# Kernel tuning notes

Hardware: AMD Instinct MI355X
Metric: run time of the kernel (lower is better)

The kernel has to match this reference:

```python
import jax, jax.numpy as jnp
import numpy as np

N_SRC, N_TGT, N_EDGES = 100000, 50000, 1000000
S_IN, T_IN, S_OUT, T_OUT = 128, 128, 64, 64
NEG_SLOPE = 0.2


def setup_inputs() -> dict:
    key = jax.random.key(0)
    ks = jax.random.split(key, 7)
    return {
        "x_source": jax.random.normal(ks[0], (N_SRC, S_IN), jnp.float32),
        "x_target": jax.random.normal(ks[1], (N_TGT, T_IN), jnp.float32),
        "w_s": jax.random.normal(ks[2], (S_IN, T_OUT), jnp.float32) * 0.1,
        "w_t": jax.random.normal(ks[3], (T_IN, S_OUT), jnp.float32) * 0.1,
        "att_weight": jax.random.normal(ks[4], (T_OUT + S_OUT,), jnp.float32) * 0.1,
        "nbhd_values": jnp.ones((N_EDGES,), jnp.float32),
        "rows": jax.random.randint(ks[5], (N_EDGES,), 0, N_TGT, jnp.int32),  # target idx i
        "cols": jax.random.randint(ks[6], (N_EDGES,), 0, N_SRC, jnp.int32),  # source idx j
    }


def reference(x_source, x_target, w_s, w_t, att_weight, nbhd_values, rows, cols):
    n_src, n_tgt = x_source.shape[0], x_target.shape[0]
    t_out = w_s.shape[1]  # dim of s_message
    s_out = w_t.shape[1]  # dim of t_message

    s_msg = x_source @ w_s  # [n_src, t_out]
    t_msg = x_target @ w_t  # [n_tgt, s_out]

    # e_{ij} = LeakyReLU([s_msg_j || t_msg_i] . a); a = [a_s (t_out) || a_t (s_out)]
    a_s, a_t = att_weight[:t_out], att_weight[t_out:]
    # f uses permuted attention vector: [a[s_out:] || a[:s_out]] on [t_msg_j || s_msg_i]
    b_t, b_s = att_weight[s_out:], att_weight[:s_out]

    es = s_msg @ a_s  # [n_src]
    et = t_msg @ a_t  # [n_tgt]
    ft = t_msg @ b_t  # [n_tgt]
    fs = s_msg @ b_s  # [n_src]

    # s->t attention: rows are target cells (row-normalize over target rows)
    e = jax.nn.leaky_relu(es[cols] + et[rows], NEG_SLOPE)  # [E]
    e_den = jax.ops.segment_sum(e, rows, num_segments=n_tgt)
    att_st = e / e_den[rows]

    # t->s attention: transposed indices; rows are source cells
    f = jax.nn.leaky_relu(ft[rows] + fs[cols], NEG_SLOPE)  # [E]
    f_den = jax.ops.segment_sum(f, cols, num_segments=n_src)
    att_ts = f / f_den[cols]

    # Hadamard with neighborhood values, then sparse-dense aggregation
    w_st = att_st * nbhd_values  # [E]
    w_ts = att_ts * nbhd_values  # [E]

    message_on_target = jax.ops.segment_sum(w_st[:, None] * s_msg[cols], rows, num_segments=n_tgt)  # [n_tgt, t_out]
    message_on_source = jax.ops.segment_sum(w_ts[:, None] * t_msg[rows], cols, num_segments=n_src)  # [n_src, s_out]

    # update_func is None -> identity
    return message_on_source, message_on_target
```

## Files before the change

### kernel.cpp

```cpp
#include <hip/hip_runtime.h>

#define N_SRC   100000
#define N_TGT   50000
#define N_EDGES 1000000
#define NEG     0.2
#define NXCD    8
#define TPART   (N_TGT / NXCD)
#define SPART   (N_SRC / NXCD)

#define GBLK_S  1563
#define GBLK_T  782
#define GBLK    (GBLK_S + GBLK_T)
#define NHIST   1280


#define XS2 65
__global__ __launch_bounds__(256) void fused_gemm_hist(
    const float* __restrict__ x_source, const float* __restrict__ x_target,
    const float* __restrict__ w_s, const float* __restrict__ w_t,
    const float* __restrict__ att,
    float* __restrict__ s_msg, float* __restrict__ t_msg,
    double* __restrict__ es_d, double* __restrict__ et_d,
    const int* __restrict__ rows, const int* __restrict__ cols,
    int* __restrict__ cnt_r, int* __restrict__ cnt_c,
    int* __restrict__ rank_r, int* __restrict__ rank_c)
{
    __shared__ float xs[64 * XS2];
    __shared__ double eds[4][64];
    const int tid = threadIdx.x;

    if (blockIdx.x < NHIST) {
        for (int i = blockIdx.x * 256 + tid; i < N_EDGES; i += NHIST * 256) {
            rank_r[i] = atomicAdd(&cnt_r[rows[i]], 1);
            rank_c[i] = atomicAdd(&cnt_c[cols[i]], 1);
        }
        return;
    }

    const int gi = blockIdx.x - NHIST;

    const float* x; const float* w; int att_off, nrows, bblk;
    float* msg; double* evec;
    if (gi < GBLK_S) { x = x_source; w = w_s; att_off = 0;  nrows = N_SRC;
                       msg = s_msg;  evec = es_d; bblk = gi; }
    else             { x = x_target; w = w_t; att_off = 64; nrows = N_TGT;
                       msg = t_msg;  evec = et_d; bblk = gi - GBLK_S; }

    const int lane = tid & 63;
    const int part = tid >> 6;
    const int c0   = __builtin_amdgcn_readfirstlane(part << 4);
    const int row0 = bblk * 64;
    const int row  = row0 + lane;
    const bool act = row < nrows;

    float acc[16];
    #pragma unroll
    for (int c = 0; c < 16; ++c) acc[c] = 0.f;

    const int xbase = lane * XS2;

    #pragma unroll
    for (int h = 0; h < 2; ++h) {
        __syncthreads();
        #pragma unroll
        for (int it = 0; it < 4; ++it) {
            const int fid = tid + it * 256;
            const int r = fid >> 4, q = fid & 15;
            if (row0 + r < nrows) {
                const float4 v =
                    *(const float4*)(x + (size_t)(row0 + r) * 128 + h * 64 + 4 * q);
                float* d = &xs[r * XS2 + 4 * q];
                d[0] = v.x; d[1] = v.y; d[2] = v.z; d[3] = v.w;
            }
        }
        __syncthreads();

        for (int kc = 0; kc < 64; kc += 16) {
            #pragma unroll
            for (int kk = 0; kk < 16; ++kk) {
                const float xk = xs[xbase + kc + kk];
                const float* wr = w + (size_t)(h * 64 + kc + kk) * 64 + c0;
                #pragma unroll
                for (int c = 0; c < 16; ++c)
                    acc[c] = fmaf(xk, wr[c], acc[c]);
            }
        }
    }

    double e = 0.0;
    #pragma unroll
    for (int c = 0; c < 16; ++c)
        e += (double)acc[c] * (double)att[att_off + c0 + c];
    eds[part][lane] = e;
    __syncthreads();
    if (part == 0 && act)
        evec[row] = eds[0][lane] + eds[1][lane] + eds[2][lane] + eds[3][lane];

    if (act) {
        float* mo = msg + (size_t)row * 64 + c0;
        #pragma unroll
        for (int q = 0; q < 4; ++q)
            *(float4*)(mo + 4 * q) = *(float4*)(acc + 4 * q);
    }
}

__global__ __launch_bounds__(1024) void scan_two(
    const int* __restrict__ cnt_r, const int* __restrict__ cnt_c,
    int* __restrict__ ptr_r, int* __restrict__ ptr_c)
{
    const int n    = blockIdx.x ? N_SRC : N_TGT;
    const int* cnt = blockIdx.x ? cnt_c : cnt_r;
    int* ptr       = blockIdx.x ? ptr_c : ptr_r;
    const int tid  = threadIdx.x;
    const int lane = tid & 63, wid = tid >> 6;

    __shared__ int wsum[16];
    __shared__ int s_carry;
    if (tid == 0) s_carry = 0;
    __syncthreads();

    for (int base = 0; base < n; base += 4096) {
        const int idx = base + tid * 4;
        int4 v = make_int4(0, 0, 0, 0);
        if (idx + 3 < n) {
            v = *(const int4*)(cnt + idx);
        } else if (idx < n) {
            v.x = cnt[idx];
            if (idx + 1 < n) v.y = cnt[idx + 1];
            if (idx + 2 < n) v.z = cnt[idx + 2];
        }
        const int s = v.x + v.y + v.z + v.w;

        int p = s;
        #pragma unroll
        for (int d = 1; d < 64; d <<= 1) {
            int t = __shfl_up(p, d);
            if (lane >= d) p += t;
        }
        if (lane == 63) wsum[wid] = p;
        __syncthreads();
        if (tid == 0) {
            int a = 0;
            #pragma unroll
            for (int i = 0; i < 16; ++i) { int t = wsum[i]; wsum[i] = a; a += t; }
        }
        __syncthreads();

        int run = s_carry + wsum[wid] + (p - s);
        if (idx     < n) ptr[idx]     = run; run += v.x;
        if (idx + 1 < n) ptr[idx + 1] = run; run += v.y;
        if (idx + 2 < n) ptr[idx + 2] = run; run += v.z;
        if (idx + 3 < n) ptr[idx + 3] = run; run += v.w;

        __syncthreads();
        if (tid == 1023) s_carry = run;
        __syncthreads();
    }
    if (tid == 0) ptr[n] = s_carry;
}

__global__ __launch_bounds__(256) void scatter_part(
    const int* __restrict__ rows, const int* __restrict__ cols,
    const float* __restrict__ nbhd,
    const int* __restrict__ ptr_r, const int* __restrict__ ptr_c,
    const int* __restrict__ rank_r, const int* __restrict__ rank_c,
    unsigned long long* __restrict__ srtT, unsigned long long* __restrict__ srtS)
{
    const int xcd  = blockIdx.x & (NXCD - 1);
    const int ibx  = blockIdx.x >> 3;
    const int step = (gridDim.x >> 3) * blockDim.x;
    const int lo_r = xcd * TPART, lo_c = xcd * SPART;

    for (int i = ibx * blockDim.x + threadIdx.x; i < N_EDGES; i += step) {
        const int r = rows[i], c = cols[i];
        const bool mr = (unsigned)(r - lo_r) < TPART;
        const bool mc = (unsigned)(c - lo_c) < SPART;
        if (!(mr | mc)) continue;
        const unsigned long long nb =
            (unsigned long long)(unsigned)__float_as_int(nbhd[i]) << 32;
        if (mr) srtT[ptr_r[r] + rank_r[i]] = nb | (unsigned)c;
        if (mc) srtS[ptr_c[c] + rank_c[i]] = nb | (unsigned)r;
    }
}

__global__ __launch_bounds__(256) void gather_both(
    const int2* __restrict__ srtT, const int* __restrict__ ptr_r,
    const float* __restrict__ s_msg, float* __restrict__ msg_tgt,
    const int2* __restrict__ srtS, const int* __restrict__ ptr_c,
    const float* __restrict__ t_msg, float* __restrict__ msg_src,
    const double* __restrict__ es_d, const double* __restrict__ et_d)
{
    const int gw   = (blockIdx.x * blockDim.x + threadIdx.x) >> 6;
    const int lane = threadIdx.x & 63;

    const int2* srt; const int* ptr; const float* min_; float* out;
    const double* other_d; double base; int row;
    if (gw < N_TGT) {
        srt = srtT; ptr = ptr_r; min_ = s_msg; out = msg_tgt;
        other_d = es_d; row = gw; base = et_d[row];
    } else {
        row = gw - N_TGT;
        if (row >= N_SRC) return;
        srt = srtS; ptr = ptr_c; min_ = t_msg; out = msg_src;
        other_d = et_d; base = es_d[row];
    }

    const int b = ptr[row], e = ptr[row + 1];
    double den = 0.0;
    float a0 = 0.f, a1 = 0.f, a2 = 0.f, a3 = 0.f;

    for (int j0 = b; j0 < e; j0 += 64) {
        const int m = e - j0;
        int oidx = 0; double v = 0.0; float wf = 0.f;
        if (lane < m) {
            const int2 pay = srt[j0 + lane];
            oidx = pay.x;
            const float nb = __int_as_float(pay.y);
            const double sv = base + other_d[oidx];
            v = (sv >= 0.0) ? sv : NEG * sv;
            wf = (float)(v * (double)nb);
        }
        den += v;

        const int cnt = m < 64 ? m : 64;
        int j = 0;
        for (; j + 3 < cnt; j += 4) {
            const int   c0_ = __shfl(oidx, j);     const float w0 = __shfl(wf, j);
            const int   c1_ = __shfl(oidx, j + 1); const float w1 = __shfl(wf, j + 1);
            const int   c2_ = __shfl(oidx, j + 2); const float w2 = __shfl(wf, j + 2);
            const int   c3_ = __shfl(oidx, j + 3); const float w3 = __shfl(wf, j + 3);
            a0 = fmaf(w0, min_[(size_t)c0_ * 64 + lane], a0);
            a1 = fmaf(w1, min_[(size_t)c1_ * 64 + lane], a1);
            a2 = fmaf(w2, min_[(size_t)c2_ * 64 + lane], a2);
            a3 = fmaf(w3, min_[(size_t)c3_ * 64 + lane], a3);
        }
        for (; j < cnt; ++j) {
            const int   c = __shfl(oidx, j);
            const float w = __shfl(wf, j);
            a0 = fmaf(w, min_[(size_t)c * 64 + lane], a0);
        }
    }
    #pragma unroll
    for (int s = 32; s; s >>= 1) den += __shfl_xor(den, s);
    const double inv = (den != 0.0) ? 1.0 / den : 0.0;
    const double acc = (double)((a0 + a1) + (a2 + a3));
    out[(size_t)row * 64 + lane] = (float)(acc * inv);
}

extern "C" void kernel_launch(void* const* d_in, const int* in_sizes, int n_in,
                              void* d_out, int out_size, void* d_ws, size_t ws_size,
                              hipStream_t stream)
{
    const float* x_source = (const float*)d_in[0];
    const float* x_target = (const float*)d_in[1];
    const float* w_s      = (const float*)d_in[2];
    const float* w_t      = (const float*)d_in[3];
    const float* att      = (const float*)d_in[4];
    const float* nbhd     = (const float*)d_in[5];
    const int*   rows     = (const int*)d_in[6];
    const int*   cols     = (const int*)d_in[7];

    float* out     = (float*)d_out;
    float* msg_src = out;
    float* msg_tgt = out + (size_t)N_SRC * 64;

    char* ws = (char*)d_ws;
    float*  s_msg  = (float*) (ws + 0);
    float*  t_msg  = (float*) (ws + 25600000);
    double* es_d   = (double*)(ws + 38400000);
    double* et_d   = (double*)(ws + 39200000);
    int*    cnt_r  = (int*)   (ws + 39600000);
    int*    cnt_c  = (int*)   (ws + 39800000);
    int*    ptr_r  = (int*)   (ws + 40200000);
    int*    ptr_c  = (int*)   (ws + 40400004);
    int*    rank_r = (int*)   (ws + 40800016);
    int*    rank_c = (int*)   (ws + 44800016);
    unsigned long long* srtT = (unsigned long long*)(ws + 48800016);
    unsigned long long* srtS = (unsigned long long*)(ws + 56800016);

    hipMemsetAsync(ws + 39600000, 0, 600000, stream);

    fused_gemm_hist<<<NHIST + GBLK, 256, 0, stream>>>(
        x_source, x_target, w_s, w_t, att,
        s_msg, t_msg, es_d, et_d,
        rows, cols, cnt_r, cnt_c, rank_r, rank_c);

    scan_two<<<2, 1024, 0, stream>>>(cnt_r, cnt_c, ptr_r, ptr_c);
    scatter_part<<<2048, 256, 0, stream>>>(
        rows, cols, nbhd, ptr_r, ptr_c, rank_r, rank_c, srtT, srtS);

    gather_both<<<(N_TGT + N_SRC + 3) / 4, 256, 0, stream>>>(
        (const int2*)srtT, ptr_r, s_msg, msg_tgt,
        (const int2*)srtS, ptr_c, t_msg, msg_src, es_d, et_d);
}
```

Baseline: 297.5 us.

## Prefetch second GEMM half, unroll histogram atomics, and use nontemporal payload loads

The histogram blocks are halved, and each thread now issues four edges' loads and atomics before storing ranks, which gives more memory-level parallelism per thread. The GEMM path prefetches the second 64-column half of each x row into registers while the first half is being computed, so the global load latency between halves is hidden. The gather kernel reads the sorted payload as 64-bit nontemporal loads to avoid polluting the cache. In exchange, the GEMM blocks use more registers and the histogram has fewer blocks to hide atomic latency.

```diff
diff --git a/kernel.cpp b/kernel.cpp
--- a/kernel.cpp
+++ b/kernel.cpp
@@ -11,7 +11,7 @@
 #define GBLK_S  1563
 #define GBLK_T  782
 #define GBLK    (GBLK_S + GBLK_T)
-#define NHIST   1280
+#define NHIST   640
 
 
 #define XS2 65
@@ -30,7 +30,27 @@
     const int tid = threadIdx.x;
 
     if (blockIdx.x < NHIST) {
-        for (int i = blockIdx.x * 256 + tid; i < N_EDGES; i += NHIST * 256) {
+        const int S = NHIST * 256;
+        int i = blockIdx.x * 256 + tid;
+        for (; i + 3 * S < N_EDGES; i += 4 * S) {
+            const int r0 = rows[i],         c0_ = cols[i];
+            const int r1 = rows[i + S],     c1_ = cols[i + S];
+            const int r2 = rows[i + 2 * S], c2_ = cols[i + 2 * S];
+            const int r3 = rows[i + 3 * S], c3_ = cols[i + 3 * S];
+            const int kr0 = atomicAdd(&cnt_r[r0], 1);
+            const int kc0 = atomicAdd(&cnt_c[c0_], 1);
+            const int kr1 = atomicAdd(&cnt_r[r1], 1);
+            const int kc1 = atomicAdd(&cnt_c[c1_], 1);
+            const int kr2 = atomicAdd(&cnt_r[r2], 1);
+            const int kc2 = atomicAdd(&cnt_c[c2_], 1);
+            const int kr3 = atomicAdd(&cnt_r[r3], 1);
+            const int kc3 = atomicAdd(&cnt_c[c3_], 1);
+            rank_r[i]         = kr0; rank_c[i]         = kc0;
+            rank_r[i + S]     = kr1; rank_c[i + S]     = kc1;
+            rank_r[i + 2 * S] = kr2; rank_c[i + 2 * S] = kc2;
+            rank_r[i + 3 * S] = kr3; rank_c[i + 3 * S] = kc3;
+        }
+        for (; i < N_EDGES; i += S) {
             rank_r[i] = atomicAdd(&cnt_r[rows[i]], 1);
             rank_c[i] = atomicAdd(&cnt_c[cols[i]], 1);
         }
@@ -60,30 +80,56 @@
     const int xbase = lane * XS2;
 
     #pragma unroll
-    for (int h = 0; h < 2; ++h) {
-        __syncthreads();
+    for (int it = 0; it < 4; ++it) {
+        const int fid = tid + it * 256;
+        const int r = fid >> 4, q = fid & 15;
+        if (row0 + r < nrows) {
+            const float4 v = *(const float4*)(x + (size_t)(row0 + r) * 128 + 4 * q);
+            float* d = &xs[r * XS2 + 4 * q];
+            d[0] = v.x; d[1] = v.y; d[2] = v.z; d[3] = v.w;
+        }
+    }
+    __syncthreads();
+
+    float4 pre[4];
+    #pragma unroll
+    for (int it = 0; it < 4; ++it) {
+        const int fid = tid + it * 256;
+        const int r = fid >> 4, q = fid & 15;
+        pre[it] = (row0 + r < nrows)
+            ? *(const float4*)(x + (size_t)(row0 + r) * 128 + 64 + 4 * q)
+            : make_float4(0.f, 0.f, 0.f, 0.f);
+    }
+
+    for (int kc = 0; kc < 64; kc += 16) {
         #pragma unroll
-        for (int it = 0; it < 4; ++it) {
-            const int fid = tid + it * 256;
-            const int r = fid >> 4, q = fid & 15;
-            if (row0 + r < nrows) {
-                const float4 v =
-                    *(const float4*)(x + (size_t)(row0 + r) * 128 + h * 64 + 4 * q);
-                float* d = &xs[r * XS2 + 4 * q];
-                d[0] = v.x; d[1] = v.y; d[2] = v.z; d[3] = v.w;
-            }
-        }
-        __syncthreads();
-
-        for (int kc = 0; kc < 64; kc += 16) {
+        for (int kk = 0; kk < 16; ++kk) {
+            const float xk = xs[xbase + kc + kk];
+            const float* wr = w + (size_t)(kc + kk) * 64 + c0;
             #pragma unroll
-            for (int kk = 0; kk < 16; ++kk) {
-                const float xk = xs[xbase + kc + kk];
-                const float* wr = w + (size_t)(h * 64 + kc + kk) * 64 + c0;
-                #pragma unroll
-                for (int c = 0; c < 16; ++c)
-                    acc[c] = fmaf(xk, wr[c], acc[c]);
-            }
+            for (int c = 0; c < 16; ++c)
+                acc[c] = fmaf(xk, wr[c], acc[c]);
+        }
+    }
+    __syncthreads();
+
+    #pragma unroll
+    for (int it = 0; it < 4; ++it) {
+        const int fid = tid + it * 256;
+        const int r = fid >> 4, q = fid & 15;
+        float* d = &xs[r * XS2 + 4 * q];
+        d[0] = pre[it].x; d[1] = pre[it].y; d[2] = pre[it].z; d[3] = pre[it].w;
+    }
+    __syncthreads();
+
+    for (int kc = 0; kc < 64; kc += 16) {
+        #pragma unroll
+        for (int kk = 0; kk < 16; ++kk) {
+            const float xk = xs[xbase + kc + kk];
+            const float* wr = w + (size_t)(64 + kc + kk) * 64 + c0;
+            #pragma unroll
+            for (int c = 0; c < 16; ++c)
+                acc[c] = fmaf(xk, wr[c], acc[c]);
         }
     }
 
@@ -184,16 +230,16 @@
 }
 
 __global__ __launch_bounds__(256) void gather_both(
-    const int2* __restrict__ srtT, const int* __restrict__ ptr_r,
+    const unsigned long long* __restrict__ srtT, const int* __restrict__ ptr_r,
     const float* __restrict__ s_msg, float* __restrict__ msg_tgt,
-    const int2* __restrict__ srtS, const int* __restrict__ ptr_c,
+    const unsigned long long* __restrict__ srtS, const int* __restrict__ ptr_c,
     const float* __restrict__ t_msg, float* __restrict__ msg_src,
     const double* __restrict__ es_d, const double* __restrict__ et_d)
 {
     const int gw   = (blockIdx.x * blockDim.x + threadIdx.x) >> 6;
     const int lane = threadIdx.x & 63;
 
-    const int2* srt; const int* ptr; const float* min_; float* out;
+    const unsigned long long* srt; const int* ptr; const float* min_; float* out;
     const double* other_d; double base; int row;
     if (gw < N_TGT) {
         srt = srtT; ptr = ptr_r; min_ = s_msg; out = msg_tgt;
@@ -213,9 +259,9 @@
         const int m = e - j0;
         int oidx = 0; double v = 0.0; float wf = 0.f;
         if (lane < m) {
-            const int2 pay = srt[j0 + lane];
-            oidx = pay.x;
-            const float nb = __int_as_float(pay.y);
+            const unsigned long long pv = __builtin_nontemporal_load(&srt[j0 + lane]);
+            oidx = (int)(unsigned)(pv & 0xFFFFFFFFull);
+            const float nb = __int_as_float((int)(unsigned)(pv >> 32));
             const double sv = base + other_d[oidx];
             v = (sv >= 0.0) ? sv : NEG * sv;
             wf = (float)(v * (double)nb);
@@ -290,6 +336,6 @@
         rows, cols, nbhd, ptr_r, ptr_c, rank_r, rank_c, srtT, srtS);
 
     gather_both<<<(N_TGT + N_SRC + 3) / 4, 256, 0, stream>>>(
-        (const int2*)srtT, ptr_r, s_msg, msg_tgt,
-        (const int2*)srtS, ptr_c, t_msg, msg_src, es_d, et_d);
-}
+        srtT, ptr_r, s_msg, msg_tgt,
+        srtS, ptr_c, t_msg, msg_src, es_d, et_d);
+}
```

New measurement: 296.4 us. No clear change (-0.4%).
